# Kernel optimization log

Hardware: AMD Instinct MI355X
Metric: run time of the kernel (lower is better)

## Reference

```python
import jax, jax.numpy as jnp
import numpy as np

B = 2; D = 256; NH = 8; NL = 4; HD = D // NH
K = 2; P = K * K; NV = 4; DFF = 1024
SHAPES = ((128, 128), (64, 64), (32, 32), (16, 16))
LV = sum(h * w for h, w in SHAPES)
START = np.cumsum([0] + [h * w for h, w in SHAPES])[:-1].tolist()
EPS = 1e-5

# fixed 2x2 sampling kernel, matching _create_kernel_indices (even kernel branch)
_ind = np.linspace(-0.5, 0.5, K)
_ii, _jj = np.meshgrid(_ind, _ind, indexing='ij')
KERNEL = jnp.asarray(np.stack([_jj, _ii], -1).reshape(-1, 2) / K, jnp.float32)  # (P,2)


def _layer_norm(x, w, b):
    m = x.mean(-1, keepdims=True)
    v = ((x - m) ** 2).mean(-1, keepdims=True)
    return (x - m) * jax.lax.rsqrt(v + EPS) * w + b


def _box_attention(query, value, ref_windows, vpw, vpb, opw, opb, boxw, boxb, attw, attb):
    b, lq, _ = query.shape
    # value projection, split into heads: (b, NH, LV, HD)
    v = (value @ vpw.T + vpb).reshape(b, LV, NH, HD).transpose(0, 2, 1, 3)

    # attention weights: softmax over all (level, point) jointly per head
    aw = query @ attw.T + attb
    aw = jax.nn.softmax(aw.reshape(b, lq, NH, NL * P), -1).reshape(b, lq, NH, NL, P)

    # where to attend (with_rotation=False -> 4 offset variables, angle from ref)
    ob = (query @ boxw.T + boxb).reshape(b, lq, NH, NL, NV)
    rw = ref_windows[:, :, None, None, :]                    # (b,lq,1,1,7)
    ref_boxes = rw[..., jnp.array([0, 1, 3, 4])]
    angles = jnp.broadcast_to(rw[..., 6:7], (b, lq, NH, NL, 1))
    boxes = ref_boxes + ob / 8.0 * ref_boxes[..., jnp.array([2, 3, 2, 3])]
    center = boxes[..., None, :2]                            # (b,lq,NH,NL,1,2)
    size = boxes[..., None, 2:]
    c, s = jnp.cos(angles), jnp.sin(angles)
    rot = jnp.stack([c, -s, s, c], -1).reshape(b, lq, NH, NL, 1, 2, 2)
    g = KERNEL * jax.nn.relu(size)                           # (b,lq,NH,NL,P,2)
    grid = center + (g[..., None, :] * rot).sum(-1)          # (b,lq,NH,NL,P,2)

    # multi-level bilinear sampling (= grid_sample align_corners=False, zero pad)
    bidx = jnp.arange(b)[:, None, None, None]
    hidx = jnp.arange(NH)[None, None, :, None]
    out = jnp.zeros((b, lq, NH, HD), v.dtype)
    for lvl, (H, W) in enumerate(SHAPES):
        st = START[lvl]
        vl = v[:, :, st:st + H * W]                          # (b,NH,HW,HD)
        loc = grid[:, :, :, lvl]                             # (b,lq,NH,P,2)
        x = loc[..., 0] * W - 0.5
        y = loc[..., 1] * H - 0.5
        x0f = jnp.floor(x); y0f = jnp.floor(y)
        wx = x - x0f; wy = y - y0f
        x0 = x0f.astype(jnp.int32); y0 = y0f.astype(jnp.int32)
        acc = jnp.zeros((b, lq, NH, P, HD), v.dtype)
        corners = ((0, 0, (1 - wx) * (1 - wy)), (1, 0, wx * (1 - wy)),
                   (0, 1, (1 - wx) * wy), (1, 1, wx * wy))
        for dx, dy, wgt in corners:
            xi = x0 + dx; yi = y0 + dy
            valid = (xi >= 0) & (xi < W) & (yi >= 0) & (yi < H)
            idx = jnp.clip(yi, 0, H - 1) * W + jnp.clip(xi, 0, W - 1)
            samp = vl[bidx, hidx, idx]                       # (b,lq,NH,P,HD)
            acc = acc + (wgt * valid)[..., None] * samp
        out = out + jnp.einsum('blhp,blhpd->blhd', aw[:, :, :, lvl], acc)
    return out.reshape(b, lq, D) @ opw.T + opb


def setup_inputs() -> dict:
    key = jax.random.key(0)
    ks = jax.random.split(key, 20)
    def nrm(k, shape, fan_in):
        return jax.random.normal(k, shape, jnp.float32) * (1.0 / np.sqrt(fan_in))
    rw = jax.random.uniform(ks[2], (B, LV, 7), jnp.float32)
    # keep window sizes (cols 3,4,5) modest, like real BEV reference windows
    rw = rw.at[..., 3:6].multiply(0.2)
    return {
        'src': jax.random.normal(ks[0], (B, LV, D), jnp.float32),
        'pos': jax.random.normal(ks[1], (B, LV, D), jnp.float32),
        'src_shape': jnp.asarray(SHAPES, jnp.int32),
        'src_start_idx': jnp.asarray(START, jnp.int32),
        'ref_windows': rw,
        'vpw': nrm(ks[3], (D, D), D), 'vpb': jnp.zeros((D,), jnp.float32),
        'opw': nrm(ks[4], (D, D), D), 'opb': jnp.zeros((D,), jnp.float32),
        'boxw': nrm(ks[5], (NL * NH * NV, D), D) * 0.1,
        'boxb': jax.random.normal(ks[6], (NL * NH * NV,), jnp.float32) * 0.1,
        'attw': nrm(ks[7], (NH * NL * P, D), D),
        'attb': jnp.zeros((NH * NL * P,), jnp.float32),
        'lin1_w': nrm(ks[8], (DFF, D), D), 'lin1_b': jnp.zeros((DFF,), jnp.float32),
        'lin2_w': nrm(ks[9], (D, DFF), DFF), 'lin2_b': jnp.zeros((D,), jnp.float32),
        'ln1_w': jnp.ones((D,), jnp.float32), 'ln1_b': jnp.zeros((D,), jnp.float32),
        'ln2_w': jnp.ones((D,), jnp.float32), 'ln2_b': jnp.zeros((D,), jnp.float32),
    }


def reference(src, pos, src_shape, src_start_idx, ref_windows,
              vpw, vpb, opw, opb, boxw, boxb, attw, attb,
              lin1_w, lin1_b, lin2_w, lin2_b, ln1_w, ln1_b, ln2_w, ln2_b):
    # level shapes/starts are static (SHAPES/START constants); src_shape /
    # src_start_idx are accepted for signature fidelity.
    src2 = _box_attention(src + pos, src, ref_windows,
                          vpw, vpb, opw, opb, boxw, boxb, attw, attb)
    src = _layer_norm(src + src2, ln1_w, ln1_b)
    ffn = jax.nn.relu(src @ lin1_w.T + lin1_b) @ lin2_w.T + lin2_b
    return _layer_norm(src + ffn, ln2_w, ln2_b)
```

## Files before the change

kernel.cpp:

```cpp
#include <hip/hip_runtime.h>
#include <stdint.h>

typedef unsigned short u16;
typedef __attribute__((ext_vector_type(8))) short short8;
typedef __attribute__((ext_vector_type(4))) float f32x4;

#define D_    256
#define NH_   8
#define HD_   32
#define LV_   21760
#define DFF_  1024
#define EPS_  1e-5f
#define MH_   21760
#define MT_   43520

__device__ __forceinline__ float bf2f(u16 u) {
    union { uint32_t i; float f; } x; x.i = ((uint32_t)u) << 16; return x.f;
}
__device__ __forceinline__ u16 f2bf(float f) {
    union { float f; uint32_t i; } x; x.f = f;
    uint32_t r = x.i + 0x7FFFu + ((x.i >> 16) & 1u);
    return (u16)(r >> 16);
}
__device__ __forceinline__ uint32_t pk2(float a, float b) {
    return (uint32_t)f2bf(a) | ((uint32_t)f2bf(b) << 16);
}
__device__ __forceinline__ float blo(uint32_t u) {
    union { uint32_t i; float f; } x; x.i = u << 16; return x.f;
}
__device__ __forceinline__ float bhi(uint32_t u) {
    union { uint32_t i; float f; } x; x.i = u & 0xffff0000u; return x.f;
}
__device__ __forceinline__ void cv8(u16* dst, float4 a, float4 b) {
    uint4 r;
    r.x = pk2(a.x, a.y); r.y = pk2(a.z, a.w);
    r.z = pk2(b.x, b.y); r.w = pk2(b.z, b.w);
    *(uint4*)dst = r;
}
__device__ __forceinline__ void cv8add(u16* dst, float4 a, float4 a2, float4 b, float4 b2) {
    uint4 r;
    r.x = pk2(a.x + a2.x, a.y + a2.y); r.y = pk2(a.z + a2.z, a.w + a2.w);
    r.z = pk2(b.x + b2.x, b.y + b2.y); r.w = pk2(b.z + b2.z, b.w + b2.w);
    *(uint4*)dst = r;
}

__global__ __launch_bounds__(256) void k_cvt(const float* __restrict__ in,
                                             u16* __restrict__ out, int n4) {
    int i = blockIdx.x * 256 + threadIdx.x;
    if (i < n4) {
        float4 v = ((const float4*)in)[i];
        uint2 r; r.x = pk2(v.x, v.y); r.y = pk2(v.z, v.w);
        *(uint2*)(out + (size_t)i * 4) = r;
    }
}

__global__ __launch_bounds__(256) void k_vprojm(
        const float* __restrict__ src, const float* __restrict__ vpw,
        const float* __restrict__ vpb, u16* __restrict__ vout) {
    __shared__ u16 As[2][64 * 32];
    __shared__ u16 Bs[2][64 * 32];
    const int t = threadIdx.x;
    const int l = t & 63, w = t >> 6;
    const int m0 = blockIdx.x * 64, n0 = blockIdx.y * 64;
    const int sr = t >> 2, sc = t & 3;
    const int wslot = sr * 32 + ((sc ^ ((sr >> 1) & 3)) << 3);
    const float* gA = src + (size_t)(m0 + sr) * 256 + sc * 8;
    const float* gB = vpw + (size_t)(n0 + sr) * 256 + sc * 8;
    const int fr = l & 15, fg = l >> 4;
    const int wm = w >> 1, wn = w & 1;

    f32x4 acc[2][2];
    #pragma unroll
    for (int mi = 0; mi < 2; ++mi)
        #pragma unroll
        for (int ni = 0; ni < 2; ++ni)
            acc[mi][ni] = (f32x4){0.f, 0.f, 0.f, 0.f};

    cv8(&As[0][wslot], *(const float4*)gA, *(const float4*)(gA + 4));
    cv8(&Bs[0][wslot], *(const float4*)gB, *(const float4*)(gB + 4));
    __syncthreads();

    for (int kt = 0; kt < 8; ++kt) {
        const int cur = kt & 1;
        float4 na0, na1, nb0, nb1;
        if (kt < 7) {
            na0 = *(const float4*)(gA + (kt + 1) * 32);
            na1 = *(const float4*)(gA + (kt + 1) * 32 + 4);
            nb0 = *(const float4*)(gB + (kt + 1) * 32);
            nb1 = *(const float4*)(gB + (kt + 1) * 32 + 4);
        }
        short8 af[2], bfr[2];
        #pragma unroll
        for (int mi = 0; mi < 2; ++mi) {
            const int r = wm * 32 + mi * 16 + fr;
            af[mi] = *(const short8*)&As[cur][r * 32 + ((fg ^ ((r >> 1) & 3)) << 3)];
        }
        #pragma unroll
        for (int ni = 0; ni < 2; ++ni) {
            const int r = wn * 32 + ni * 16 + fr;
            bfr[ni] = *(const short8*)&Bs[cur][r * 32 + ((fg ^ ((r >> 1) & 3)) << 3)];
        }
        #pragma unroll
        for (int mi = 0; mi < 2; ++mi)
            #pragma unroll
            for (int ni = 0; ni < 2; ++ni)
                acc[mi][ni] = __builtin_amdgcn_mfma_f32_16x16x32_bf16(af[mi], bfr[ni], acc[mi][ni], 0, 0, 0);
        if (kt < 7) {
            cv8(&As[cur ^ 1][wslot], na0, na1);
            cv8(&Bs[cur ^ 1][wslot], nb0, nb1);
            __syncthreads();
        }
    }
    const int b = m0 / LV_;
    #pragma unroll
    for (int ni = 0; ni < 2; ++ni) {
        const int n = n0 + wn * 32 + ni * 16 + fr;
        const float bv = vpb[n];
        const int h = n >> 5, hd = n & 31;
        #pragma unroll
        for (int mi = 0; mi < 2; ++mi) {
            #pragma unroll
            for (int q = 0; q < 4; ++q) {
                const int m = m0 + wm * 32 + mi * 16 + fg * 4 + q;
                const int lrow = m - b * LV_;
                vout[((size_t)(b * NH_ + h) * LV_ + lrow) * HD_ + hd] = f2bf(acc[mi][ni][q] + bv);
            }
        }
    }
}

__global__ __launch_bounds__(256) void k_logits(
        const float* __restrict__ src, const float* __restrict__ pos,
        const float* __restrict__ attw, const float* __restrict__ attb,
        const float* __restrict__ boxw, const float* __restrict__ boxb,
        float* __restrict__ logits) {
    __shared__ u16 As[2][64 * 32];
    __shared__ u16 Bs[2][64 * 32];
    const int t = threadIdx.x;
    const int l = t & 63, w = t >> 6;
    const int m0 = blockIdx.x * 64;
    const int n0g = blockIdx.y * 64;
    const float* Bsrc = (n0g < 128) ? (attw + (size_t)n0g * 256) : (boxw + (size_t)(n0g - 128) * 256);
    const float* bsrc = (n0g < 128) ? (attb + n0g) : (boxb + (n0g - 128));
    const int sr = t >> 2, sc = t & 3;
    const int wslot = sr * 32 + ((sc ^ ((sr >> 1) & 3)) << 3);
    const float* gAs = src + (size_t)(m0 + sr) * 256 + sc * 8;
    const float* gAp = pos + (size_t)(m0 + sr) * 256 + sc * 8;
    const float* gB  = Bsrc + (size_t)sr * 256 + sc * 8;
    const int fr = l & 15, fg = l >> 4;
    const int wm = w >> 1, wn = w & 1;

    f32x4 acc[2][2];
    #pragma unroll
    for (int mi = 0; mi < 2; ++mi)
        #pragma unroll
        for (int ni = 0; ni < 2; ++ni)
            acc[mi][ni] = (f32x4){0.f, 0.f, 0.f, 0.f};

    cv8add(&As[0][wslot], *(const float4*)gAs, *(const float4*)gAp,
                          *(const float4*)(gAs + 4), *(const float4*)(gAp + 4));
    cv8(&Bs[0][wslot], *(const float4*)gB, *(const float4*)(gB + 4));
    __syncthreads();

    for (int kt = 0; kt < 8; ++kt) {
        const int cur = kt & 1;
        float4 ns0, ns1, np0, np1, nb0, nb1;
        if (kt < 7) {
            ns0 = *(const float4*)(gAs + (kt + 1) * 32);
            ns1 = *(const float4*)(gAs + (kt + 1) * 32 + 4);
            np0 = *(const float4*)(gAp + (kt + 1) * 32);
            np1 = *(const float4*)(gAp + (kt + 1) * 32 + 4);
            nb0 = *(const float4*)(gB + (kt + 1) * 32);
            nb1 = *(const float4*)(gB + (kt + 1) * 32 + 4);
        }
        short8 af[2], bfr[2];
        #pragma unroll
        for (int mi = 0; mi < 2; ++mi) {
            const int r = wm * 32 + mi * 16 + fr;
            af[mi] = *(const short8*)&As[cur][r * 32 + ((fg ^ ((r >> 1) & 3)) << 3)];
        }
        #pragma unroll
        for (int ni = 0; ni < 2; ++ni) {
            const int r = wn * 32 + ni * 16 + fr;
            bfr[ni] = *(const short8*)&Bs[cur][r * 32 + ((fg ^ ((r >> 1) & 3)) << 3)];
        }
        #pragma unroll
        for (int mi = 0; mi < 2; ++mi)
            #pragma unroll
            for (int ni = 0; ni < 2; ++ni)
                acc[mi][ni] = __builtin_amdgcn_mfma_f32_16x16x32_bf16(af[mi], bfr[ni], acc[mi][ni], 0, 0, 0);
        if (kt < 7) {
            cv8add(&As[cur ^ 1][wslot], ns0, np0, ns1, np1);
            cv8(&Bs[cur ^ 1][wslot], nb0, nb1);
            __syncthreads();
        }
    }
    #pragma unroll
    for (int ni = 0; ni < 2; ++ni) {
        const int nl_ = wn * 32 + ni * 16 + fr;
        const float bv = bsrc[nl_];
        #pragma unroll
        for (int mi = 0; mi < 2; ++mi) {
            #pragma unroll
            for (int q = 0; q < 4; ++q) {
                const int m = m0 + wm * 32 + mi * 16 + fg * 4 + q;
                logits[(size_t)m * 256 + n0g + nl_] = acc[mi][ni][q] + bv;
            }
        }
    }
}

__global__ __launch_bounds__(256) void k_sample(
        const float* __restrict__ logits, const float* __restrict__ refw,
        const u16* __restrict__ vws, u16* __restrict__ smp) {
    __shared__ float AWL[8][128];
    __shared__ float OBL[8][128];
    __shared__ __align__(16) uint2 CWI[128 * 18];
    __shared__ float RW[8][8];
    const int t = threadIdx.x;
    const int bid = blockIdx.x;
    const int sb = (bid & 7) * (gridDim.x >> 3) + (bid >> 3);
    const long gr0 = (long)sb * 8;
    const int b = (int)(gr0 / LV_);
    {
        const float4* lp = (const float4*)(logits + gr0 * 256);
        #pragma unroll
        for (int i = 0; i < 2; ++i) {
            int ii = t + i * 256;
            float4 v = lp[ii];
            int r = ii >> 6, c4 = (ii & 63) << 2;
            if (c4 < 128) *(float4*)&AWL[r][c4] = v;
            else          *(float4*)&OBL[r][c4 - 128] = v;
        }
        if (t < 56) {
            int r2 = t / 7, k = t % 7;
            RW[r2][k] = refw[(gr0 + r2) * 7 + k];
        }
    }
    __syncthreads();
    if (t < 64) {
        const int r = t >> 3, h = t & 7;
        float* a = &AWL[r][h * 16];
        float m = a[0];
        #pragma unroll
        for (int k = 1; k < 16; ++k) m = fmaxf(m, a[k]);
        float s = 0.f;
        float e[16];
        #pragma unroll
        for (int k = 0; k < 16; ++k) { e[k] = __expf(a[k] - m); s += e[k]; }
        const float inv = 1.f / s;
        #pragma unroll
        for (int k = 0; k < 16; ++k) a[k] = e[k] * inv;
    }
    __syncthreads();

    const int e = t & 7;
    const int g = t >> 3;
    const int rloc_g = g & 3, hg = g >> 2;
    const char* vbp = (const char*)vws +
        (((size_t)(b * NH_ + hg) * LV_) * HD_ + e * 4) * 2;
    const int cu = t & 127, rsel = t >> 7;
    const int ch = cu >> 4, cnl = (cu >> 2) & 3, cp = cu & 3;

    for (int wdw = 0; wdw < 2; ++wdw) {
        #pragma unroll
        for (int rr = 0; rr < 2; ++rr) {
            const int rloc = rsel * 2 + rr;
            const int row = wdw * 4 + rloc;
            const float rw0 = RW[row][0], rw1 = RW[row][1], rw3 = RW[row][3], rw4 = RW[row][4], ang = RW[row][6];
            const int obb = ch * 16 + cnl * 4;
            const float ob0 = OBL[row][obb + 0];
            const float ob1 = OBL[row][obb + 1];
            const float ob2 = OBL[row][obb + 2];
            const float ob3 = OBL[row][obb + 3];
            const float cx = rw0 + ob0 * 0.125f * rw3;
            const float cy = rw1 + ob1 * 0.125f * rw4;
            const float bw = fmaxf(rw3 + ob2 * 0.125f * rw3, 0.f);
            const float bh = fmaxf(rw4 + ob3 * 0.125f * rw4, 0.f);
            const float kx = (cp & 1) ? 0.25f : -0.25f;
            const float ky = (cp >> 1) ? 0.25f : -0.25f;
            float sth, cth;
            __sincosf(ang, &sth, &cth);
            const float g0 = kx * bw, g1 = ky * bh;
            const float gx = cx + g0 * cth - g1 * sth;
            const float gy = cy + g0 * sth + g1 * cth;
            const int Wl = 128 >> cnl;
            const int st = (65536 - (65536 >> (2 * cnl))) / 3;
            const float x = gx * Wl - 0.5f, y = gy * Wl - 0.5f;
            const float xf = floorf(x), yf = floorf(y);
            const float wx = x - xf, wy = y - yf;
            const int x0 = (int)xf, y0 = (int)yf;
            const float awv = AWL[row][cu];
            uint2 cw[4];
            #pragma unroll
            for (int c4 = 0; c4 < 4; ++c4) {
                const int dx = c4 & 1, dy = c4 >> 1;
                const int xi = x0 + dx, yi = y0 + dy;
                const float wgt = (dx ? wx : 1.f - wx) * (dy ? wy : 1.f - wy);
                const bool valid = (xi >= 0) && (xi < Wl) && (yi >= 0) && (yi < Wl);
                const int xc = xi < 0 ? 0 : (xi > Wl - 1 ? Wl - 1 : xi);
                const int yc = yi < 0 ? 0 : (yi > Wl - 1 ? Wl - 1 : yi);
                const float wv = valid ? wgt * awv : 0.f;
                cw[c4].x = __float_as_uint(wv);
                cw[c4].y = (uint32_t)(st + yc * Wl + xc) * 64u;
            }
            uint2* dst = &CWI[cu * 18 + rloc * 4];
            *(uint4*)(dst)     = *(const uint4*)&cw[0];
            *(uint4*)(dst + 2) = *(const uint4*)&cw[2];
        }
        __syncthreads();
        {
            const int row = wdw * 4 + rloc_g;
            float a0 = 0.f, a1 = 0.f, a2 = 0.f, a3 = 0.f;
            #pragma unroll 4
            for (int k = 0; k < 16; ++k) {
                const int ub = (hg * 16 + k) * 18 + rloc_g * 4;
                #pragma unroll
                for (int cc = 0; cc < 2; ++cc) {
                    const uint4 cw2 = *(const uint4*)&CWI[ub + cc * 2];
                    const float w0 = __uint_as_float(cw2.x);
                    const uint2 d0 = *(const uint2*)(vbp + cw2.y);
                    const float w1 = __uint_as_float(cw2.z);
                    const uint2 d1 = *(const uint2*)(vbp + cw2.w);
                    a0 += w0 * blo(d0.x); a1 += w0 * bhi(d0.x);
                    a2 += w0 * blo(d0.y); a3 += w0 * bhi(d0.y);
                    a0 += w1 * blo(d1.x); a1 += w1 * bhi(d1.x);
                    a2 += w1 * blo(d1.y); a3 += w1 * bhi(d1.y);
                }
            }
            uint2 o; o.x = pk2(a0, a1); o.y = pk2(a2, a3);
            *(uint2*)(smp + (size_t)(gr0 + row) * 256 + hg * 32 + e * 4) = o;
        }
        __syncthreads();
    }
}

__global__ __launch_bounds__(256) void k_oproj(
        const u16* __restrict__ A,
        const float* __restrict__ opw,
        const float* __restrict__ opb,
        const float* __restrict__ src,
        const float* __restrict__ lnw, const float* __restrict__ lnb,
        u16* __restrict__ out) {
    __shared__ char smem[36864];
    u16* As = (u16*)smem;
    u16* Bs = (u16*)(smem + 4096);
    float* Y = (float*)smem;
    const int t = threadIdx.x;
    const int l = t & 63, w = t >> 6;
    const int m0 = blockIdx.x * 32;
    const int sAr = t >> 2, sc = t & 3;
    const int aslot = sAr * 32 + ((sc ^ ((sAr >> 1) & 3)) << 3);
    const u16* gA = A + (size_t)(m0 + sAr) * 256 + sc * 8;
    const float* gB[4];
    int bslot[4];
    #pragma unroll
    for (int i = 0; i < 4; ++i) {
        const int r = (t >> 2) + i * 64;
        gB[i] = opw + (size_t)r * 256 + sc * 8;
        bslot[i] = r * 32 + ((sc ^ ((r >> 1) & 3)) << 3);
    }
    const int fr = l & 15, fg = l >> 4;

    f32x4 acc[2][4];
    #pragma unroll
    for (int mi = 0; mi < 2; ++mi)
        #pragma unroll
        for (int ni = 0; ni < 4; ++ni)
            acc[mi][ni] = (f32x4){0.f, 0.f, 0.f, 0.f};

    if (t < 128) *(uint4*)&As[aslot] = *(const uint4*)gA;
    #pragma unroll
    for (int i = 0; i < 4; ++i)
        cv8(&Bs[bslot[i]], *(const float4*)gB[i], *(const float4*)(gB[i] + 4));
    __syncthreads();

    for (int kt = 0; kt < 8; ++kt) {
        const int cur = kt & 1;
        uint4 na; float4 nb[4][2];
        if (kt < 7) {
            if (t < 128) na = *(const uint4*)(gA + (kt + 1) * 32);
            #pragma unroll
            for (int i = 0; i < 4; ++i) {
                nb[i][0] = *(const float4*)(gB[i] + (kt + 1) * 32);
                nb[i][1] = *(const float4*)(gB[i] + (kt + 1) * 32 + 4);
            }
        }
        short8 af[2], bfr[4];
        #pragma unroll
        for (int mi = 0; mi < 2; ++mi) {
            const int r = mi * 16 + fr;
            af[mi] = *(const short8*)&As[cur * 1024 + r * 32 + ((fg ^ ((r >> 1) & 3)) << 3)];
        }
        #pragma unroll
        for (int ni = 0; ni < 4; ++ni) {
            const int r = w * 64 + ni * 16 + fr;
            bfr[ni] = *(const short8*)&Bs[cur * 8192 + r * 32 + ((fg ^ ((r >> 1) & 3)) << 3)];
        }
        #pragma unroll
        for (int mi = 0; mi < 2; ++mi)
            #pragma unroll
            for (int ni = 0; ni < 4; ++ni)
                acc[mi][ni] = __builtin_amdgcn_mfma_f32_16x16x32_bf16(af[mi], bfr[ni], acc[mi][ni], 0, 0, 0);
        if (kt < 7) {
            if (t < 128) *(uint4*)&As[(cur ^ 1) * 1024 + aslot] = na;
            #pragma unroll
            for (int i = 0; i < 4; ++i)
                cv8(&Bs[(cur ^ 1) * 8192 + bslot[i]], nb[i][0], nb[i][1]);
            __syncthreads();
        }
    }
    __syncthreads();
    #pragma unroll
    for (int ni = 0; ni < 4; ++ni) {
        const int n = w * 64 + ni * 16 + fr;
        const float bv = opb[n];
        #pragma unroll
        for (int mi = 0; mi < 2; ++mi) {
            #pragma unroll
            for (int q = 0; q < 4; ++q) {
                const int ml = mi * 16 + fg * 4 + q;
                Y[ml * 256 + n] = acc[mi][ni][q] + bv + src[(size_t)(m0 + ml) * 256 + n];
            }
        }
    }
    __syncthreads();
    for (int rr = 0; rr < 8; ++rr) {
        const int m = w * 8 + rr;
        const float v0 = Y[m * 256 + l];
        const float v1 = Y[m * 256 + 64 + l];
        const float v2 = Y[m * 256 + 128 + l];
        const float v3 = Y[m * 256 + 192 + l];
        float s1 = v0 + v1 + v2 + v3;
        float s2 = v0 * v0 + v1 * v1 + v2 * v2 + v3 * v3;
        #pragma unroll
        for (int off = 32; off; off >>= 1) {
            s1 += __shfl_xor(s1, off);
            s2 += __shfl_xor(s2, off);
        }
        const float mean = s1 * (1.f / 256.f);
        const float var = s2 * (1.f / 256.f) - mean * mean;
        const float rs = rsqrtf(var + EPS_);
        const size_t ob = (size_t)(m0 + m) * 256;
        out[ob + l]       = f2bf((v0 - mean) * rs * lnw[l]       + lnb[l]);
        out[ob + 64 + l]  = f2bf((v1 - mean) * rs * lnw[64 + l]  + lnb[64 + l]);
        out[ob + 128 + l] = f2bf((v2 - mean) * rs * lnw[128 + l] + lnb[128 + l]);
        out[ob + 192 + l] = f2bf((v3 - mean) * rs * lnw[192 + l] + lnb[192 + l]);
    }
}

__global__ __launch_bounds__(256) void k_gemm1(
        const u16* __restrict__ A, const u16* __restrict__ Bw,
        const float* __restrict__ bias, u16* __restrict__ H) {
    __shared__ u16 As[2][128 * 32];
    __shared__ u16 Bs[2][128 * 32];
    const int t = threadIdx.x;
    const int l = t & 63, w = t >> 6;
    const int m0 = blockIdx.x * 128, n0 = blockIdx.y * 128;
    const int sr = t >> 1, sc0 = (t & 1) * 2;
    const int ws0 = sr * 32 + ((sc0 ^ ((sr >> 1) & 3)) << 3);
    const int ws1 = sr * 32 + (((sc0 + 1) ^ ((sr >> 1) & 3)) << 3);
    const u16* gA = A + (size_t)(m0 + sr) * 256 + sc0 * 8;
    const u16* gB = Bw + (size_t)(n0 + sr) * 256 + sc0 * 8;
    const int fr = l & 15, fg = l >> 4;
    const int wm = w >> 1, wn = w & 1;

    f32x4 acc[4][4];
    #pragma unroll
    for (int mi = 0; mi < 4; ++mi)
        #pragma unroll
        for (int ni = 0; ni < 4; ++ni)
            acc[mi][ni] = (f32x4){0.f, 0.f, 0.f, 0.f};

    *(uint4*)&As[0][ws0] = *(const uint4*)(gA);
    *(uint4*)&As[0][ws1] = *(const uint4*)(gA + 8);
    *(uint4*)&Bs[0][ws0] = *(const uint4*)(gB);
    *(uint4*)&Bs[0][ws1] = *(const uint4*)(gB + 8);
    __syncthreads();

    for (int kt = 0; kt < 8; ++kt) {
        const int cur = kt & 1;
        uint4 na0, na1, nb0, nb1;
        if (kt < 7) {
            na0 = *(const uint4*)(gA + (kt + 1) * 32);
            na1 = *(const uint4*)(gA + (kt + 1) * 32 + 8);
            nb0 = *(const uint4*)(gB + (kt + 1) * 32);
            nb1 = *(const uint4*)(gB + (kt + 1) * 32 + 8);
        }
        short8 af[4], bfr[4];
        #pragma unroll
        for (int mi = 0; mi < 4; ++mi) {
            const int r = wm * 64 + mi * 16 + fr;
            af[mi] = *(const short8*)&As[cur][r * 32 + ((fg ^ ((r >> 1) & 3)) << 3)];
        }
        #pragma unroll
        for (int ni = 0; ni < 4; ++ni) {
            const int r = wn * 64 + ni * 16 + fr;
            bfr[ni] = *(const short8*)&Bs[cur][r * 32 + ((fg ^ ((r >> 1) & 3)) << 3)];
        }
        #pragma unroll
        for (int mi = 0; mi < 4; ++mi)
            #pragma unroll
            for (int ni = 0; ni < 4; ++ni)
                acc[mi][ni] = __builtin_amdgcn_mfma_f32_16x16x32_bf16(af[mi], bfr[ni], acc[mi][ni], 0, 0, 0);
        if (kt < 7) {
            *(uint4*)&As[cur ^ 1][ws0] = na0;
            *(uint4*)&As[cur ^ 1][ws1] = na1;
            *(uint4*)&Bs[cur ^ 1][ws0] = nb0;
            *(uint4*)&Bs[cur ^ 1][ws1] = nb1;
            __syncthreads();
        }
    }
    #pragma unroll
    for (int ni = 0; ni < 4; ++ni) {
        const int n = n0 + wn * 64 + ni * 16 + fr;
        const float bv = bias[n];
        #pragma unroll
        for (int mi = 0; mi < 4; ++mi) {
            #pragma unroll
            for (int q = 0; q < 4; ++q) {
                const int m = m0 + wm * 64 + mi * 16 + fg * 4 + q;
                const float v = acc[mi][ni][q] + bv;
                H[(size_t)m * 1024 + n] = f2bf(fmaxf(v, 0.f));
            }
        }
    }
}

__global__ __launch_bounds__(256) void k_gemm2(
        const u16* __restrict__ A, const u16* __restrict__ Bw,
        const float* __restrict__ bias, const u16* __restrict__ resid,
        const float* __restrict__ lnw, const float* __restrict__ lnb,
        float* __restrict__ out) {
    __shared__ char smem[36864];
    u16* As = (u16*)smem;
    u16* Bs = (u16*)(smem + 4096);
    float* Y = (float*)smem;
    const int t = threadIdx.x;
    const int l = t & 63, w = t >> 6;
    const int m0 = blockIdx.x * 32;
    const int sAr = t >> 2, sc = t & 3;
    const int aslot = sAr * 32 + ((sc ^ ((sAr >> 1) & 3)) << 3);
    const u16* gA = A + (size_t)(m0 + sAr) * 1024 + sc * 8;
    const u16* gB[4];
    int bslot[4];
    #pragma unroll
    for (int i = 0; i < 4; ++i) {
        const int r = (t >> 2) + i * 64;
        gB[i] = Bw + (size_t)r * 1024 + sc * 8;
        bslot[i] = r * 32 + ((sc ^ ((r >> 1) & 3)) << 3);
    }
    const int fr = l & 15, fg = l >> 4;

    f32x4 acc[2][4];
    #pragma unroll
    for (int mi = 0; mi < 2; ++mi)
        #pragma unroll
        for (int ni = 0; ni < 4; ++ni)
            acc[mi][ni] = (f32x4){0.f, 0.f, 0.f, 0.f};

    if (t < 128) *(uint4*)&As[aslot] = *(const uint4*)(gA);
    #pragma unroll
    for (int i = 0; i < 4; ++i) *(uint4*)&Bs[bslot[i]] = *(const uint4*)(gB[i]);
    __syncthreads();

    for (int kt = 0; kt < 32; ++kt) {
        const int cur = kt & 1;
        uint4 na, nb[4];
        if (kt < 31) {
            if (t < 128) na = *(const uint4*)(gA + (kt + 1) * 32);
            #pragma unroll
            for (int i = 0; i < 4; ++i) nb[i] = *(const uint4*)(gB[i] + (kt + 1) * 32);
        }
        short8 af[2], bfr[4];
        #pragma unroll
        for (int mi = 0; mi < 2; ++mi) {
            const int r = mi * 16 + fr;
            af[mi] = *(const short8*)&As[cur * 1024 + r * 32 + ((fg ^ ((r >> 1) & 3)) << 3)];
        }
        #pragma unroll
        for (int ni = 0; ni < 4; ++ni) {
            const int r = w * 64 + ni * 16 + fr;
            bfr[ni] = *(const short8*)&Bs[cur * 8192 + r * 32 + ((fg ^ ((r >> 1) & 3)) << 3)];
        }
        #pragma unroll
        for (int mi = 0; mi < 2; ++mi)
            #pragma unroll
            for (int ni = 0; ni < 4; ++ni)
                acc[mi][ni] = __builtin_amdgcn_mfma_f32_16x16x32_bf16(af[mi], bfr[ni], acc[mi][ni], 0, 0, 0);
        if (kt < 31) {
            if (t < 128) *(uint4*)&As[(cur ^ 1) * 1024 + aslot] = na;
            #pragma unroll
            for (int i = 0; i < 4; ++i) *(uint4*)&Bs[(cur ^ 1) * 8192 + bslot[i]] = nb[i];
            __syncthreads();
        }
    }
    __syncthreads();
    #pragma unroll
    for (int ni = 0; ni < 4; ++ni) {
        const int n = w * 64 + ni * 16 + fr;
        const float bv = bias[n];
        #pragma unroll
        for (int mi = 0; mi < 2; ++mi) {
            #pragma unroll
            for (int q = 0; q < 4; ++q) {
                const int ml = mi * 16 + fg * 4 + q;
                Y[ml * 256 + n] = acc[mi][ni][q] + bv + bf2f(resid[(size_t)(m0 + ml) * 256 + n]);
            }
        }
    }
    __syncthreads();
    for (int rr = 0; rr < 8; ++rr) {
        const int m = w * 8 + rr;
        const float v0 = Y[m * 256 + l];
        const float v1 = Y[m * 256 + 64 + l];
        const float v2 = Y[m * 256 + 128 + l];
        const float v3 = Y[m * 256 + 192 + l];
        float s1 = v0 + v1 + v2 + v3;
        float s2 = v0 * v0 + v1 * v1 + v2 * v2 + v3 * v3;
        #pragma unroll
        for (int off = 32; off; off >>= 1) {
            s1 += __shfl_xor(s1, off);
            s2 += __shfl_xor(s2, off);
        }
        const float mean = s1 * (1.f / 256.f);
        const float var = s2 * (1.f / 256.f) - mean * mean;
        const float rs = rsqrtf(var + EPS_);
        const size_t ob = (size_t)(m0 + m) * 256;
        out[ob + l]        = (v0 - mean) * rs * lnw[l]        + lnb[l];
        out[ob + 64 + l]   = (v1 - mean) * rs * lnw[64 + l]   + lnb[64 + l];
        out[ob + 128 + l]  = (v2 - mean) * rs * lnw[128 + l]  + lnb[128 + l];
        out[ob + 192 + l]  = (v3 - mean) * rs * lnw[192 + l]  + lnb[192 + l];
    }
}

extern "C" void kernel_launch(void* const* d_in, const int* in_sizes, int n_in,
                              void* d_out, int out_size, void* d_ws, size_t ws_size,
                              hipStream_t stream) {
    const float* src  = (const float*)d_in[0];
    const float* pos  = (const float*)d_in[1];
    const float* refw = (const float*)d_in[4];
    const float* vpw  = (const float*)d_in[5];
    const float* vpb  = (const float*)d_in[6];
    const float* opw  = (const float*)d_in[7];
    const float* opb  = (const float*)d_in[8];
    const float* boxw = (const float*)d_in[9];
    const float* boxb = (const float*)d_in[10];
    const float* attw = (const float*)d_in[11];
    const float* attb = (const float*)d_in[12];
    const float* l1w  = (const float*)d_in[13];
    const float* l1b  = (const float*)d_in[14];
    const float* l2w  = (const float*)d_in[15];
    const float* l2b  = (const float*)d_in[16];
    const float* ln1w = (const float*)d_in[17];
    const float* ln1b = (const float*)d_in[18];
    const float* ln2w = (const float*)d_in[19];
    const float* ln2b = (const float*)d_in[20];

    u16*   vws    = (u16*)d_ws;
    u16*   l1wb   = (u16*)d_ws;
    u16*   l2wb   = (u16*)((char*)d_ws + 524288);
    float* logits = (float*)((char*)d_ws + 22282240u);
    u16*   src1b  = (u16*)((char*)d_ws + 22282240u);
    u16*   Hbf    = (u16*)((char*)d_ws + 44564480u);
    u16*   smp    = (u16*)((char*)d_ws + 66846720u);

    hipLaunchKernelGGL(k_vprojm, dim3(680, 4), dim3(256), 0, stream, src, vpw, vpb, vws);
    hipLaunchKernelGGL(k_logits, dim3(680, 4), dim3(256), 0, stream,
                       src, pos, attw, attb, boxw, boxb, logits);
    hipLaunchKernelGGL(k_sample, dim3(5440), dim3(256), 0, stream, logits, refw, vws, smp);
    hipLaunchKernelGGL(k_cvt, dim3(256), dim3(256), 0, stream, l1w, l1wb, 65536);
    hipLaunchKernelGGL(k_cvt, dim3(256), dim3(256), 0, stream, l2w, l2wb, 65536);
    hipLaunchKernelGGL(k_oproj, dim3(1360), dim3(256), 0, stream,
                       smp, opw, opb, src, ln1w, ln1b, src1b);
    for (int h = 0; h < 2; ++h) {
        const u16* Ah = src1b + (size_t)h * MH_ * 256;
        float* outh   = (float*)d_out + (size_t)h * MH_ * 256;
        hipLaunchKernelGGL(k_gemm1, dim3(170, 8), dim3(256), 0, stream, Ah, l1wb, l1b, Hbf);
        hipLaunchKernelGGL(k_gemm2, dim3(680), dim3(256), 0, stream, Hbf, l2wb, l2b, Ah, ln2w, ln2b, outh);
    }
}
```

Before: 356.5 us.

## Store logits as bf16 in head-interleaved layout; split sampling blocks by head pair

The logits GEMM now writes bf16 instead of fp32 and interleaves attention and box offset columns per head, so each head's 32 values sit contiguously. The sampling kernel is reorganised so each block handles 16 rows for one batch and one pair of heads, with grid index bits selecting batch and head pair. The two-window loop and its extra barriers are removed, and each block reads only its heads' logits. This halves logits traffic and should improve locality of the value gathers per head, at the cost of bf16 rounding on softmax logits and box offsets, and twice as many blocks.

```diff
diff --git a/kernel.cpp b/kernel.cpp
--- a/kernel.cpp
+++ b/kernel.cpp
@@ -133,7 +133,7 @@
         const float* __restrict__ src, const float* __restrict__ pos,
         const float* __restrict__ attw, const float* __restrict__ attb,
         const float* __restrict__ boxw, const float* __restrict__ boxb,
-        float* __restrict__ logits) {
+        u16* __restrict__ lgout) {
     __shared__ u16 As[2][64 * 32];
     __shared__ u16 Bs[2][64 * 32];
     const int t = threadIdx.x;
@@ -198,49 +198,52 @@
     #pragma unroll
     for (int ni = 0; ni < 2; ++ni) {
         const int nl_ = wn * 32 + ni * 16 + fr;
+        const int n = n0g + nl_;
         const float bv = bsrc[nl_];
+        const int off = (n < 128) ? ((n >> 4) * 32 + (n & 15))
+                                  : (((n - 128) >> 4) * 32 + 16 + ((n - 128) & 15));
         #pragma unroll
         for (int mi = 0; mi < 2; ++mi) {
             #pragma unroll
             for (int q = 0; q < 4; ++q) {
                 const int m = m0 + wm * 32 + mi * 16 + fg * 4 + q;
-                logits[(size_t)m * 256 + n0g + nl_] = acc[mi][ni][q] + bv;
+                lgout[(size_t)m * 256 + off] = f2bf(acc[mi][ni][q] + bv);
             }
         }
     }
 }
 
 __global__ __launch_bounds__(256) void k_sample(
-        const float* __restrict__ logits, const float* __restrict__ refw,
+        const u16* __restrict__ lg, const float* __restrict__ refw,
         const u16* __restrict__ vws, u16* __restrict__ smp) {
-    __shared__ float AWL[8][128];
-    __shared__ float OBL[8][128];
-    __shared__ __align__(16) uint2 CWI[128 * 18];
-    __shared__ float RW[8][8];
+    __shared__ float LG[16][2][32];
+    __shared__ float RW[16][8];
+    __shared__ __align__(16) uint2 CWI[32 * 66];
     const int t = threadIdx.x;
     const int bid = blockIdx.x;
-    const int sb = (bid & 7) * (gridDim.x >> 3) + (bid >> 3);
-    const long gr0 = (long)sb * 8;
-    const int b = (int)(gr0 / LV_);
+    const int combo = bid & 7;
+    const int idx = bid >> 3;
+    const int b = combo >> 2, hp = combo & 3;
+    const int h0 = hp * 2;
+    const long gr0 = (long)b * LV_ + (long)idx * 16;
+
     {
-        const float4* lp = (const float4*)(logits + gr0 * 256);
-        #pragma unroll
-        for (int i = 0; i < 2; ++i) {
-            int ii = t + i * 256;
-            float4 v = lp[ii];
-            int r = ii >> 6, c4 = (ii & 63) << 2;
-            if (c4 < 128) *(float4*)&AWL[r][c4] = v;
-            else          *(float4*)&OBL[r][c4 - 128] = v;
-        }
-        if (t < 56) {
+        const int row = t >> 4, part = t & 15;
+        const uint2 v = *(const uint2*)(lg + (size_t)(gr0 + row) * 256 + h0 * 32 + part * 4);
+        const int hs = part >> 3, kk = (part & 7) * 4;
+        LG[row][hs][kk]     = blo(v.x);
+        LG[row][hs][kk + 1] = bhi(v.x);
+        LG[row][hs][kk + 2] = blo(v.y);
+        LG[row][hs][kk + 3] = bhi(v.y);
+        if (t < 112) {
             int r2 = t / 7, k = t % 7;
             RW[r2][k] = refw[(gr0 + r2) * 7 + k];
         }
     }
     __syncthreads();
-    if (t < 64) {
-        const int r = t >> 3, h = t & 7;
-        float* a = &AWL[r][h * 16];
+    if (t < 32) {
+        const int row = t >> 1, hs = t & 1;
+        float* a = LG[row][hs];
         float m = a[0];
         #pragma unroll
         for (int k = 1; k < 16; ++k) m = fmaxf(m, a[k]);
@@ -253,85 +256,76 @@
         for (int k = 0; k < 16; ++k) a[k] = e[k] * inv;
     }
     __syncthreads();
-
-    const int e = t & 7;
-    const int g = t >> 3;
-    const int rloc_g = g & 3, hg = g >> 2;
-    const char* vbp = (const char*)vws +
-        (((size_t)(b * NH_ + hg) * LV_) * HD_ + e * 4) * 2;
-    const int cu = t & 127, rsel = t >> 7;
-    const int ch = cu >> 4, cnl = (cu >> 2) & 3, cp = cu & 3;
-
-    for (int wdw = 0; wdw < 2; ++wdw) {
-        #pragma unroll
-        for (int rr = 0; rr < 2; ++rr) {
-            const int rloc = rsel * 2 + rr;
-            const int row = wdw * 4 + rloc;
-            const float rw0 = RW[row][0], rw1 = RW[row][1], rw3 = RW[row][3], rw4 = RW[row][4], ang = RW[row][6];
-            const int obb = ch * 16 + cnl * 4;
-            const float ob0 = OBL[row][obb + 0];
-            const float ob1 = OBL[row][obb + 1];
-            const float ob2 = OBL[row][obb + 2];
-            const float ob3 = OBL[row][obb + 3];
-            const float cx = rw0 + ob0 * 0.125f * rw3;
-            const float cy = rw1 + ob1 * 0.125f * rw4;
-            const float bw = fmaxf(rw3 + ob2 * 0.125f * rw3, 0.f);
-            const float bh = fmaxf(rw4 + ob3 * 0.125f * rw4, 0.f);
-            const float kx = (cp & 1) ? 0.25f : -0.25f;
-            const float ky = (cp >> 1) ? 0.25f : -0.25f;
-            float sth, cth;
-            __sincosf(ang, &sth, &cth);
-            const float g0 = kx * bw, g1 = ky * bh;
-            const float gx = cx + g0 * cth - g1 * sth;
-            const float gy = cy + g0 * sth + g1 * cth;
-            const int Wl = 128 >> cnl;
-            const int st = (65536 - (65536 >> (2 * cnl))) / 3;
-            const float x = gx * Wl - 0.5f, y = gy * Wl - 0.5f;
-            const float xf = floorf(x), yf = floorf(y);
-            const float wx = x - xf, wy = y - yf;
-            const int x0 = (int)xf, y0 = (int)yf;
-            const float awv = AWL[row][cu];
-            uint2 cw[4];
-            #pragma unroll
-            for (int c4 = 0; c4 < 4; ++c4) {
-                const int dx = c4 & 1, dy = c4 >> 1;
-                const int xi = x0 + dx, yi = y0 + dy;
-                const float wgt = (dx ? wx : 1.f - wx) * (dy ? wy : 1.f - wy);
-                const bool valid = (xi >= 0) && (xi < Wl) && (yi >= 0) && (yi < Wl);
-                const int xc = xi < 0 ? 0 : (xi > Wl - 1 ? Wl - 1 : xi);
-                const int yc = yi < 0 ? 0 : (yi > Wl - 1 ? Wl - 1 : yi);
-                const float wv = valid ? wgt * awv : 0.f;
-                cw[c4].x = __float_as_uint(wv);
-                cw[c4].y = (uint32_t)(st + yc * Wl + xc) * 64u;
+    #pragma unroll
+    for (int uu = 0; uu < 2; ++uu) {
+        const int u = t + uu * 256;
+        const int row = u >> 5, rem = u & 31;
+        const int hs = rem >> 4, nl = (rem >> 2) & 3, p = rem & 3;
+        const float rw0 = RW[row][0], rw1 = RW[row][1], rw3 = RW[row][3], rw4 = RW[row][4], ang = RW[row][6];
+        const float ob0 = LG[row][hs][16 + nl * 4 + 0];
+        const float ob1 = LG[row][hs][16 + nl * 4 + 1];
+        const float ob2 = LG[row][hs][16 + nl * 4 + 2];
+        const float ob3 = LG[row][hs][16 + nl * 4 + 3];
+        const float cx = rw0 + ob0 * 0.125f * rw3;
+        const float cy = rw1 + ob1 * 0.125f * rw4;
+        const float bw = fmaxf(rw3 + ob2 * 0.125f * rw3, 0.f);
+        const float bh = fmaxf(rw4 + ob3 * 0.125f * rw4, 0.f);
+        const float kx = (p & 1) ? 0.25f : -0.25f;
+        const float ky = (p >> 1) ? 0.25f : -0.25f;
+        float sth, cth;
+        __sincosf(ang, &sth, &cth);
+        const float g0 = kx * bw, g1 = ky * bh;
+        const float gx = cx + g0 * cth - g1 * sth;
+        const float gy = cy + g0 * sth + g1 * cth;
+        const int Wl = 128 >> nl;
+        const int st = (65536 - (65536 >> (2 * nl))) / 3;
+        const float x = gx * Wl - 0.5f, y = gy * Wl - 0.5f;
+        const float xf = floorf(x), yf = floorf(y);
+        const float wx = x - xf, wy = y - yf;
+        const int x0 = (int)xf, y0 = (int)yf;
+        const float awv = LG[row][hs][nl * 4 + p];
+        uint2 cw[4];
+        #pragma unroll
+        for (int c4 = 0; c4 < 4; ++c4) {
+            const int dx = c4 & 1, dy = c4 >> 1;
+            const int xi = x0 + dx, yi = y0 + dy;
+            const float wgt = (dx ? wx : 1.f - wx) * (dy ? wy : 1.f - wy);
+            const bool valid = (xi >= 0) && (xi < Wl) && (yi >= 0) && (yi < Wl);
+            const int xc = xi < 0 ? 0 : (xi > Wl - 1 ? Wl - 1 : xi);
+            const int yc = yi < 0 ? 0 : (yi > Wl - 1 ? Wl - 1 : yi);
+            const float wv = valid ? wgt * awv : 0.f;
+            cw[c4].x = __float_as_uint(wv);
+            cw[c4].y = (uint32_t)(st + yc * Wl + xc) * 64u;
+        }
+        uint2* dst = &CWI[(row * 2 + hs) * 66 + (nl * 4 + p) * 4];
+        *(uint4*)(dst)     = *(const uint4*)&cw[0];
+        *(uint4*)(dst + 2) = *(const uint4*)&cw[2];
+    }
+    __syncthreads();
+    {
+        const int e = t & 7, g = t >> 3;
+        const int row = g >> 1, hs = g & 1, h = h0 + hs;
+        const char* vbp = (const char*)vws +
+            (((size_t)(b * NH_ + h) * LV_) * HD_ + e * 4) * 2;
+        const uint2* cbase = &CWI[g * 66];
+        float a0 = 0.f, a1 = 0.f, a2 = 0.f, a3 = 0.f;
+        #pragma unroll 4
+        for (int k = 0; k < 16; ++k) {
+            #pragma unroll
+            for (int cc = 0; cc < 2; ++cc) {
+                const uint4 cw2 = *(const uint4*)&cbase[k * 4 + cc * 2];
+                const float w0 = __uint_as_float(cw2.x);
+                const uint2 d0 = *(const uint2*)(vbp + cw2.y);
+                const float w1 = __uint_as_float(cw2.z);
+                const uint2 d1 = *(const uint2*)(vbp + cw2.w);
+                a0 += w0 * blo(d0.x); a1 += w0 * bhi(d0.x);
+                a2 += w0 * blo(d0.y); a3 += w0 * bhi(d0.y);
+                a0 += w1 * blo(d1.x); a1 += w1 * bhi(d1.x);
+                a2 += w1 * blo(d1.y); a3 += w1 * bhi(d1.y);
             }
-            uint2* dst = &CWI[cu * 18 + rloc * 4];
-            *(uint4*)(dst)     = *(const uint4*)&cw[0];
-            *(uint4*)(dst + 2) = *(const uint4*)&cw[2];
-        }
-        __syncthreads();
-        {
-            const int row = wdw * 4 + rloc_g;
-            float a0 = 0.f, a1 = 0.f, a2 = 0.f, a3 = 0.f;
-            #pragma unroll 4
-            for (int k = 0; k < 16; ++k) {
-                const int ub = (hg * 16 + k) * 18 + rloc_g * 4;
-                #pragma unroll
-                for (int cc = 0; cc < 2; ++cc) {
-                    const uint4 cw2 = *(const uint4*)&CWI[ub + cc * 2];
-                    const float w0 = __uint_as_float(cw2.x);
-                    const uint2 d0 = *(const uint2*)(vbp + cw2.y);
-                    const float w1 = __uint_as_float(cw2.z);
-                    const uint2 d1 = *(const uint2*)(vbp + cw2.w);
-                    a0 += w0 * blo(d0.x); a1 += w0 * bhi(d0.x);
-                    a2 += w0 * blo(d0.y); a3 += w0 * bhi(d0.y);
-                    a0 += w1 * blo(d1.x); a1 += w1 * bhi(d1.x);
-                    a2 += w1 * blo(d1.y); a3 += w1 * bhi(d1.y);
-                }
-            }
-            uint2 o; o.x = pk2(a0, a1); o.y = pk2(a2, a3);
-            *(uint2*)(smp + (size_t)(gr0 + row) * 256 + hg * 32 + e * 4) = o;
-        }
-        __syncthreads();
+        }
+        uint2 o; o.x = pk2(a0, a1); o.y = pk2(a2, a3);
+        *(uint2*)(smp + (size_t)(gr0 + row) * 256 + h * 32 + e * 4) = o;
     }
 }
 
@@ -660,15 +654,15 @@
     u16*   vws    = (u16*)d_ws;
     u16*   l1wb   = (u16*)d_ws;
     u16*   l2wb   = (u16*)((char*)d_ws + 524288);
-    float* logits = (float*)((char*)d_ws + 22282240u);
+    u16*   logitsb= (u16*)((char*)d_ws + 22282240u);
     u16*   src1b  = (u16*)((char*)d_ws + 22282240u);
     u16*   Hbf    = (u16*)((char*)d_ws + 44564480u);
     u16*   smp    = (u16*)((char*)d_ws + 66846720u);
 
     hipLaunchKernelGGL(k_vprojm, dim3(680, 4), dim3(256), 0, stream, src, vpw, vpb, vws);
     hipLaunchKernelGGL(k_logits, dim3(680, 4), dim3(256), 0, stream,
-                       src, pos, attw, attb, boxw, boxb, logits);
-    hipLaunchKernelGGL(k_sample, dim3(5440), dim3(256), 0, stream, logits, refw, vws, smp);
+                       src, pos, attw, attb, boxw, boxb, logitsb);
+    hipLaunchKernelGGL(k_sample, dim3(10880), dim3(256), 0, stream, logitsb, refw, vws, smp);
     hipLaunchKernelGGL(k_cvt, dim3(256), dim3(256), 0, stream, l1w, l1wb, 65536);
     hipLaunchKernelGGL(k_cvt, dim3(256), dim3(256), 0, stream, l2w, l2wb, 65536);
     hipLaunchKernelGGL(k_oproj, dim3(1360), dim3(256), 0, stream,
```

Result: faster. 320.8 us (-10.0%).
